# Kernel tuning notes

Measured on AMD Instinct MI355X. Metric: run time of the kernel, lower is better.

Reference implementation:

```python
import jax, jax.numpy as jnp
import numpy as np
import math

NP, MNP, BS, DIM, NH, TOPK, FF = 512, 4096, 8, 256, 8, 32, 2048
HD = DIM // NH
EPS = 1e-5


def _ln(x, w, b):
    mu = jnp.mean(x, axis=-1, keepdims=True)
    var = jnp.mean((x - mu) ** 2, axis=-1, keepdims=True)
    return (x - mu) / jnp.sqrt(var + EPS) * w + b


def _lin(x, w, b):
    return x @ w.T + b


def setup_inputs() -> dict:
    key = jax.random.key(0)
    ks = jax.random.split(key, 16)
    s = 0.02
    d = {
        "tgt": jax.random.normal(ks[0], (NP, BS, DIM), jnp.float32),
        "memory": jax.random.normal(ks[1], (MNP, BS, DIM), jnp.float32),
        "query_pos": jax.random.normal(ks[2], (NP, BS, DIM), jnp.float32),
        "key_pos": jax.random.normal(ks[3], (MNP, BS, DIM), jnp.float32),
        "cw1": jax.random.normal(ks[4], (DIM, DIM), jnp.float32) * s,
        "cb1": jnp.zeros((DIM,), jnp.float32),
        "cw2": jax.random.normal(ks[5], (DIM, DIM), jnp.float32) * s,
        "cb2": jnp.zeros((DIM,), jnp.float32),
        "cw3": jax.random.normal(ks[6], (DIM, DIM), jnp.float32) * s,
        "cb3": jnp.zeros((DIM,), jnp.float32),
        "sa_in_w": jax.random.normal(ks[7], (3 * DIM, DIM), jnp.float32) * s,
        "sa_in_b": jnp.zeros((3 * DIM,), jnp.float32),
        "sa_out_w": jax.random.normal(ks[8], (DIM, DIM), jnp.float32) * s,
        "sa_out_b": jnp.zeros((DIM,), jnp.float32),
        "ln1_w": jnp.ones((DIM,), jnp.float32),
        "ln1_b": jnp.zeros((DIM,), jnp.float32),
        "ln2_w": jnp.ones((DIM,), jnp.float32),
        "ln2_b": jnp.zeros((DIM,), jnp.float32),
        "ln3_w": jnp.ones((DIM,), jnp.float32),
        "ln3_b": jnp.zeros((DIM,), jnp.float32),
        "ff1_w": jax.random.normal(ks[9], (FF, DIM), jnp.float32) * s,
        "ff1_b": jnp.zeros((FF,), jnp.float32),
        "ff2_w": jax.random.normal(ks[10], (DIM, FF), jnp.float32) * s,
        "ff2_b": jnp.zeros((DIM,), jnp.float32),
    }
    return d


def _forward(tgt, memory, query_pos, key_pos,
             cw1, cb1, cw2, cb2, cw3, cb3,
             sa_in_w, sa_in_b, sa_out_w, sa_out_b,
             ln1_w, ln1_b, ln2_w, ln2_b, ln3_w, ln3_b,
             ff1_w, ff1_b, ff2_w, ff2_b):
    npq, bs, dim = tgt.shape
    mnp = memory.shape[0]
    scale = 1.0 / math.sqrt(HD)

    # --- top-k cosine similarity neighbor selection (indices, non-diff) ---
    x = tgt.transpose(1, 0, 2)        # [bs, np, dim]
    m = memory.transpose(1, 0, 2)     # [bs, mnp, dim]
    xn = x / jnp.linalg.norm(x, axis=2, keepdims=True)
    mn = m / jnp.linalg.norm(m, axis=2, keepdims=True)
    sim = jnp.einsum('bnd,bmd->bnm', xn, mn)          # [bs, np, mnp]
    _, rns = jax.lax.top_k(sim, TOPK)                  # [bs, np, topk]

    # --- masked cross attention ---
    qc = (tgt + query_pos).transpose(1, 0, 2)          # [bs, np, dim]
    kc = (memory + key_pos).transpose(1, 0, 2)         # [bs, mnp, dim]
    vc = m
    qh = _lin(qc, cw1, cb1).reshape(bs, npq, NH, HD).transpose(0, 2, 1, 3)   # [bs,nh,np,hd]
    kh = _lin(kc, cw2, cb2).reshape(bs, mnp, NH, HD).transpose(0, 2, 1, 3)   # [bs,nh,mnp,hd]
    vh = _lin(vc, cw3, cb3).reshape(bs, mnp, NH, HD).transpose(0, 2, 1, 3)   # [bs,nh,mnp,hd]
    w = jnp.einsum('bhnd,bhmd->bhnm', qh, kh) * scale                         # [bs,nh,np,mnp]

    b_idx = jnp.arange(bs)[:, None, None]
    n_idx = jnp.arange(npq)[None, :, None]
    mask = jnp.zeros((bs, npq, mnp), w.dtype).at[b_idx, n_idx, rns].set(1.0)  # same for all heads
    mask = mask[:, None, :, :]                                                # [bs,1,np,mnp]
    w = w * mask + (-1e9) * (1.0 - mask)
    w = jax.nn.softmax(w, axis=3)
    cross = jnp.einsum('bhnm,bhmd->bhnd', w, vh).transpose(2, 0, 1, 3).reshape(npq, bs, dim)

    t = _ln(tgt + cross, ln1_w, ln1_b)

    # --- self attention (torch nn.MultiheadAttention, q=k=t+pos, v=t) ---
    wq, wk, wv = sa_in_w[:DIM], sa_in_w[DIM:2 * DIM], sa_in_w[2 * DIM:]
    bq, bk, bv = sa_in_b[:DIM], sa_in_b[DIM:2 * DIM], sa_in_b[2 * DIM:]
    qk = t + query_pos                                 # [np, bs, dim]
    q2 = _lin(qk, wq, bq).transpose(1, 0, 2).reshape(bs, npq, NH, HD).transpose(0, 2, 1, 3)
    k2 = _lin(qk, wk, bk).transpose(1, 0, 2).reshape(bs, npq, NH, HD).transpose(0, 2, 1, 3)
    v2 = _lin(t, wv, bv).transpose(1, 0, 2).reshape(bs, npq, NH, HD).transpose(0, 2, 1, 3)
    attn = jax.nn.softmax(jnp.einsum('bhnd,bhmd->bhnm', q2, k2) * scale, axis=-1)
    sa = jnp.einsum('bhnm,bhmd->bhnd', attn, v2).transpose(2, 0, 1, 3).reshape(npq, bs, dim)
    sa = _lin(sa, sa_out_w, sa_out_b)

    t = _ln(t + sa, ln2_w, ln2_b)

    # --- FFN (exact GELU, matching torch F.gelu default) ---
    ff = _lin(jax.nn.gelu(_lin(t, ff1_w, ff1_b), approximate=False), ff2_w, ff2_b)
    t = _ln(t + ff, ln3_w, ln3_b)
    return t


def reference(tgt, memory, query_pos, key_pos,
              cw1, cb1, cw2, cb2, cw3, cb3,
              sa_in_w, sa_in_b, sa_out_w, sa_out_b,
              ln1_w, ln1_b, ln2_w, ln2_b, ln3_w, ln3_b,
              ff1_w, ff1_b, ff2_w, ff2_b):
    return _forward(tgt, memory, query_pos, key_pos,
                    cw1, cb1, cw2, cb2, cw3, cb3,
                    sa_in_w, sa_in_b, sa_out_w, sa_out_b,
                    ln1_w, ln1_b, ln2_w, ln2_b, ln3_w, ln3_b,
                    ff1_w, ff1_b, ff2_w, ff2_b)
```

## Files before the change

### kernel.cpp

```cpp
#include <hip/hip_runtime.h>
#include <math.h>

typedef unsigned short u16;
typedef unsigned int u32;
typedef __bf16 bf16x8 __attribute__((ext_vector_type(8)));
typedef float f32x4 __attribute__((ext_vector_type(4)));

#define NPQ 512
#define MNP 4096
#define BSZ 8
#define DIM 256
#define NH 8
#define HD 32
#define TOPK 32
#define FFD 2048
#define SCALE 0.17677669529663687f

__device__ __forceinline__ u16 f2bf(float f){
  u32 u = __builtin_bit_cast(u32, f);
  u = (u + 0x7FFFu + ((u >> 16) & 1u)) >> 16;
  return (u16)u;
}
__device__ __forceinline__ float bf2f(u16 h){
  u32 u = ((u32)h) << 16;
  return __builtin_bit_cast(float, u);
}
__device__ __forceinline__ float wredsum(float v){
#pragma unroll
  for (int m = 32; m; m >>= 1) v += __shfl_xor(v, m, 64);
  return v;
}
__device__ __forceinline__ float gelu_exact(float x){
  return 0.5f * x * (1.0f + erff(x * 0.70710678118654752f));
}
__device__ __forceinline__ u32 keytr(u32 u){
  return u ^ (((u32)((int)u >> 31)) | 0x80000000u);
}

__global__ __launch_bounds__(256)
void cvt_all(const float* __restrict__ s0, const float* __restrict__ s1,
             const float* __restrict__ s2, const float* __restrict__ s3,
             const float* __restrict__ s4, const float* __restrict__ s5,
             const float* __restrict__ s6, u16* __restrict__ dst){
  int i = blockIdx.x*256 + threadIdx.x;
  if (i >= 1507328) return;
  const float* s; int base;
  if      (i <  65536){ s = s0; base = 0; }
  else if (i < 131072){ s = s1; base = 65536; }
  else if (i < 196608){ s = s2; base = 131072; }
  else if (i < 393216){ s = s3; base = 196608; }
  else if (i < 458752){ s = s4; base = 393216; }
  else if (i < 983040){ s = s5; base = 458752; }
  else                { s = s6; base = 983040; }
  dst[i] = f2bf(s[i - base]);
}

__global__ __launch_bounds__(256)
void prep_tgt(const float* __restrict__ tgt, const float* __restrict__ qpos,
              u16* __restrict__ xnh, u16* __restrict__ xnl, u16* __restrict__ qc,
              const float* __restrict__ cb2, const float* __restrict__ cb3,
              float* __restrict__ cbKV){
  __shared__ float sc[4];
  int r = blockIdx.x, t = threadIdx.x;
  if (r == 0){ cbKV[t] = cb2[t]; cbKV[256 + t] = cb3[t]; }
  int b = r >> 9, n = r & 511;
  long src = ((long)n*BSZ + b)*DIM + t;
  float x = tgt[src];
  float s = wredsum(x*x);
  if ((t & 63) == 0) sc[t >> 6] = s;
  __syncthreads();
  float tot = sc[0]+sc[1]+sc[2]+sc[3];
  float xn = x / sqrtf(tot);
  u16 hi = f2bf(xn);
  long dst = (long)r*DIM + t;
  xnh[dst] = hi;
  xnl[dst] = f2bf(xn - bf2f(hi));
  qc[dst]  = f2bf(x + qpos[src]);
}

__global__ __launch_bounds__(256)
void prep_mem(const float* __restrict__ mem, const float* __restrict__ kpos,
              u16* __restrict__ mnh, u16* __restrict__ mnl,
              u16* __restrict__ kc, u16* __restrict__ vc){
  __shared__ float sc[4];
  int r = blockIdx.x, t = threadIdx.x;
  int b = r >> 12, mp = r & 4095;
  long src = ((long)mp*BSZ + b)*DIM + t;
  float x = mem[src];
  float s = wredsum(x*x);
  if ((t & 63) == 0) sc[t >> 6] = s;
  __syncthreads();
  float tot = sc[0]+sc[1]+sc[2]+sc[3];
  float xn = x / sqrtf(tot);
  u16 hi = f2bf(xn);
  long dst = (long)r*DIM + t;
  mnh[dst] = hi;
  mnl[dst] = f2bf(xn - bf2f(hi));
  kc[dst]  = f2bf(x + kpos[src]);
  vc[dst]  = f2bf(x);
}

#define BST 136
__global__ __launch_bounds__(256, 2)
void sim_gemm(const u16* __restrict__ xnh, const u16* __restrict__ xnl,
              const u16* __restrict__ mnh, const u16* __restrict__ mnl,
              float* __restrict__ sim){
  __shared__ __align__(16) u16 Bh[128*BST];
  __shared__ __align__(16) u16 Bl[128*BST];
  int t = threadIdx.x, lane = t & 63, wv = t >> 6;
  int ml = lane & 15, quad = lane >> 4;
  int b = blockIdx.z;
  int tM = blockIdx.y * 128 + (wv & 1) * 64;
  int tN = blockIdx.x * 128;
  int nloc = (wv >> 1) * 64;
  const u16* Ah = xnh + ((long)b*NPQ + tM + ml)*DIM;
  const u16* Al = xnl + ((long)b*NPQ + tM + ml)*DIM;
  f32x4 acc[4][4];
  f32x4 zer = {0.f,0.f,0.f,0.f};
#pragma unroll
  for (int i = 0; i < 4; i++)
#pragma unroll
    for (int j = 0; j < 4; j++) acc[i][j] = zer;

  int srow = t >> 4, scg = t & 15;
  for (int half = 0; half < 2; half++){
    int k0 = half * 128;
    if (half) __syncthreads();
#pragma unroll
    for (int p = 0; p < 8; p++){
      int r = p*16 + srow;
      long g = ((long)b*MNP + tN + r)*DIM + k0 + scg*8;
      *(uint4*)(&Bh[r*BST + scg*8]) = *(const uint4*)(mnh + g);
      *(uint4*)(&Bl[r*BST + scg*8]) = *(const uint4*)(mnl + g);
    }
    bf16x8 ca[4], ca2[4], na[4], na2[4];
#pragma unroll
    for (int i = 0; i < 4; i++){
      ca[i]  = *(const bf16x8*)(Ah + (long)i*16*DIM + k0 + quad*8);
      ca2[i] = *(const bf16x8*)(Al + (long)i*16*DIM + k0 + quad*8);
    }
    __syncthreads();
#pragma unroll
    for (int kk = 0; kk < 128; kk += 32){
      if (kk < 96){
#pragma unroll
        for (int i = 0; i < 4; i++){
          na[i]  = *(const bf16x8*)(Ah + (long)i*16*DIM + k0 + kk + 32 + quad*8);
          na2[i] = *(const bf16x8*)(Al + (long)i*16*DIM + k0 + kk + 32 + quad*8);
        }
      }
      bf16x8 bh[4], bl[4];
#pragma unroll
      for (int j = 0; j < 4; j++){
        int nr = nloc + j*16 + ml;
        bh[j] = *(const bf16x8*)(&Bh[nr*BST + kk + quad*8]);
        bl[j] = *(const bf16x8*)(&Bl[nr*BST + kk + quad*8]);
      }
#pragma unroll
      for (int i = 0; i < 4; i++)
#pragma unroll
        for (int j = 0; j < 4; j++){
          acc[i][j] = __builtin_amdgcn_mfma_f32_16x16x32_bf16(ca[i],  bh[j], acc[i][j], 0, 0, 0);
          acc[i][j] = __builtin_amdgcn_mfma_f32_16x16x32_bf16(ca[i],  bl[j], acc[i][j], 0, 0, 0);
          acc[i][j] = __builtin_amdgcn_mfma_f32_16x16x32_bf16(ca2[i], bh[j], acc[i][j], 0, 0, 0);
        }
#pragma unroll
      for (int i = 0; i < 4; i++){ ca[i] = na[i]; ca2[i] = na2[i]; }
    }
  }
  long zC = (long)b * NPQ * MNP;
#pragma unroll
  for (int i = 0; i < 4; i++)
#pragma unroll
    for (int r = 0; r < 4; r++){
      int row = tM + i*16 + quad*4 + r;
#pragma unroll
      for (int j = 0; j < 4; j++){
        int col = tN + nloc + j*16 + ml;
        sim[zC + (long)row*MNP + col] = acc[i][j][r];
      }
    }
}

#define PBST 264
template<int KGROUPS, int OUT_BF16, int ACT>
__global__ __launch_bounds__(256)
void pgemm(const u16* __restrict__ A, const u16* __restrict__ A2, int selCol,
           const u16* __restrict__ B, const float* __restrict__ bias,
           void* __restrict__ Cv, int N){
  __shared__ __align__(16) u16 Bs[64*PBST];
  const int K = KGROUPS*256;
  int t = threadIdx.x, lane = t & 63, wv = t >> 6;
  int ml = lane & 15, quad = lane >> 4;
  int tM = blockIdx.x*64;
  int tN = blockIdx.y*64;
  const u16* Ab = (tN < selCol) ? A : A2;
  const u16* Arow = Ab + (long)(tM + wv*16 + ml)*K;
  f32x4 acc[4];
  f32x4 zer = {0.f,0.f,0.f,0.f};
#pragma unroll
  for (int nj = 0; nj < 4; nj++) acc[nj] = zer;
  int srow = t >> 5, scol = (t & 31)*8;
  for (int g = 0; g < KGROUPS; g++){
    if (g) __syncthreads();
#pragma unroll
    for (int p = 0; p < 8; p++){
      int r = p*8 + srow;
      *(uint4*)(&Bs[r*PBST + scol]) = *(const uint4*)(B + (long)(tN + r)*K + g*256 + scol);
    }
    bf16x8 a[8];
#pragma unroll
    for (int kk = 0; kk < 8; kk++)
      a[kk] = *(const bf16x8*)(Arow + g*256 + kk*32 + quad*8);
    __syncthreads();
#pragma unroll
    for (int kk = 0; kk < 8; kk++){
#pragma unroll
      for (int nj = 0; nj < 4; nj++){
        bf16x8 bv = *(const bf16x8*)(&Bs[(nj*16 + ml)*PBST + kk*32 + quad*8]);
        acc[nj] = __builtin_amdgcn_mfma_f32_16x16x32_bf16(a[kk], bv, acc[nj], 0, 0, 0);
      }
    }
  }
#pragma unroll
  for (int nj = 0; nj < 4; nj++){
    int col = tN + nj*16 + ml;
    float bv = bias[col];
#pragma unroll
    for (int r = 0; r < 4; r++){
      int row = tM + wv*16 + quad*4 + r;
      float v = acc[nj][r] + bv;
      if (ACT == 1) v = gelu_exact(v);
      long idx = (long)row * N + col;
      if (OUT_BF16) ((u16*)Cv)[idx] = f2bf(v);
      else ((float*)Cv)[idx] = v;
    }
  }
}

#define HSTRIDE 264
__global__ __launch_bounds__(256, 4)
void topk_k(const float* __restrict__ sim, int* __restrict__ rns){
  __shared__ int hist[4*HSTRIDE];
  __shared__ int sh_B, sh_above;
  __shared__ int scnt, stcnt;
  __shared__ int sties[256];
  int t = threadIdx.x, wv = t >> 6;
  long r = blockIdx.x;
  const uint4* row4 = (const uint4*)(sim + r*4096);
  u32 key[16];
#pragma unroll
  for (int j = 0; j < 4; j++){
    uint4 v = row4[j*256 + t];
    key[j*4+0] = keytr(v.x);
    key[j*4+1] = keytr(v.y);
    key[j*4+2] = keytr(v.z);
    key[j*4+3] = keytr(v.w);
  }
#pragma unroll
  for (int i = 0; i < 16; i++) asm volatile("" : "+v"(key[i]));
  if (t == 0){ scnt = 0; stcnt = 0; }
  u32 pref = 0;
  int k_above = 0;
#pragma unroll 1
  for (int round = 0; round < 4; round++){
    int shift = 24 - round*8;
    u32 pmask = (round == 0) ? 0u : (0xFFFFFFFFu << (shift + 8));
    for (int z = t; z < 4*HSTRIDE; z += 256) hist[z] = 0;
    __syncthreads();
    int* myh = hist + wv*HSTRIDE;
#pragma unroll
    for (int i = 0; i < 16; i++){
      if (((key[i] ^ pref) & pmask) == 0)
        atomicAdd(&myh[(key[i] >> shift) & 255], 1);
    }
    __syncthreads();
    if (t < 64){
      int b0 = t*4+0, b1 = t*4+1, b2 = t*4+2, b3 = t*4+3;
      int h0 = hist[b0] + hist[HSTRIDE+b0] + hist[2*HSTRIDE+b0] + hist[3*HSTRIDE+b0];
      int h1 = hist[b1] + hist[HSTRIDE+b1] + hist[2*HSTRIDE+b1] + hist[3*HSTRIDE+b1];
      int h2 = hist[b2] + hist[HSTRIDE+b2] + hist[2*HSTRIDE+b2] + hist[3*HSTRIDE+b2];
      int h3 = hist[b3] + hist[HSTRIDE+b3] + hist[2*HSTRIDE+b3] + hist[3*HSTRIDE+b3];
      int local = h0 + h1 + h2 + h3;
      int s = local;
#pragma unroll
      for (int off = 1; off < 64; off <<= 1){
        int v = __shfl_down(s, off, 64);
        s += (t + off < 64) ? v : 0;
      }
      int excl = s - local;
      int a3 = excl, a2 = a3 + h3, a1 = a2 + h2, a0 = a1 + h1;
      int ka = k_above;
      if (ka + a3 < TOPK && ka + a3 + h3 >= TOPK){ sh_B = t*4+3; sh_above = ka + a3; }
      if (ka + a2 < TOPK && ka + a2 + h2 >= TOPK){ sh_B = t*4+2; sh_above = ka + a2; }
      if (ka + a1 < TOPK && ka + a1 + h1 >= TOPK){ sh_B = t*4+1; sh_above = ka + a1; }
      if (ka + a0 < TOPK && ka + a0 + h0 >= TOPK){ sh_B = t*4+0; sh_above = ka + a0; }
    }
    __syncthreads();
    pref |= ((u32)sh_B) << shift;
    k_above = sh_above;
  }
  int* out = rns + r*32;
#pragma unroll
  for (int i = 0; i < 16; i++){
    int gidx = (i >> 2)*1024 + t*4 + (i & 3);
    u32 kk = key[i];
    if (kk > pref){
      int p = atomicAdd(&scnt, 1);
      out[p] = gidx;
    } else if (kk == pref){
      int p = atomicAdd(&stcnt, 1);
      if (p < 256) sties[p] = gidx;
    }
  }
  __syncthreads();
  if (t == 0){
    int n = stcnt; if (n > 256) n = 256;
    int k_rem = TOPK - k_above;
    for (int s = 0; s < k_rem; s++){
      int mb = 0;
      for (int j = 1; j < n; j++) if (sties[j] < sties[mb]) mb = j;
      out[k_above + s] = sties[mb];
      sties[mb] = 0x7FFFFFFF;
    }
  }
}

#define CAS 272
__global__ __launch_bounds__(256)
void cross_attn(const u16* __restrict__ qh, const u16* __restrict__ khvh,
                const int* __restrict__ rns, float* __restrict__ crossO){
  __shared__ __align__(16) u16 Kg[32*CAS];
  __shared__ __align__(16) u16 Vg[32*CAS];
  __shared__ float qv[256];
  __shared__ int idxs[32];
  __shared__ float L[256];
  __shared__ float pm[8], ps[8];
  int r = blockIdx.x, t = threadIdx.x;
  int b = r >> 9;
  if (t < 32) idxs[t] = rns[(long)r*32 + t];
  qv[t] = bf2f(qh[(long)r*DIM + t]);
  __syncthreads();
  for (int i = t; i < 32*64; i += 256){
    int k = i >> 6, c = (i & 63) * 4;
    long src = ((long)b*MNP + idxs[k])*512 + c;
    *(ushort4*)(&Kg[k*CAS + c]) = *(const ushort4*)(khvh + src);
    *(ushort4*)(&Vg[k*CAS + c]) = *(const ushort4*)(khvh + src + 256);
  }
  __syncthreads();
  {
    int h = t >> 5, k = t & 31;
    float acc = 0.f;
#pragma unroll
    for (int d = 0; d < 32; d++) acc += qv[h*HD + d] * bf2f(Kg[k*CAS + h*HD + d]);
    L[t] = acc * SCALE;
  }
  __syncthreads();
  if (t < 8){
    float m = L[t*32];
    for (int k = 1; k < 32; k++) m = fmaxf(m, L[t*32 + k]);
    float s = 0.f;
    for (int k = 0; k < 32; k++) s += expf(L[t*32 + k] - m);
    pm[t] = m; ps[t] = s;
  }
  __syncthreads();
  {
    int h = t >> 5, dd = t & 31;
    float m = pm[h], inv = 1.0f/ps[h], acc = 0.f;
#pragma unroll
    for (int k = 0; k < 32; k++) acc += expf(L[h*32 + k] - m) * bf2f(Vg[k*CAS + h*HD + dd]);
    crossO[(long)r*DIM + t] = acc * inv;
  }
}

template<int MODE>
__global__ __launch_bounds__(256)
void ln_k(const float* __restrict__ xa, const float* __restrict__ xb,
          const float* __restrict__ qpos,
          const float* __restrict__ w, const float* __restrict__ bsh,
          float* __restrict__ yf, u16* __restrict__ yb, u16* __restrict__ qkb){
  __shared__ float sc[8];
  int r = blockIdx.x, t = threadIdx.x;
  int b = r >> 9, n = r & 511;
  long bidx = (long)r*DIM + t;
  long nidx = ((long)n*BSZ + b)*DIM + t;
  float x = (MODE == 1 ? xa[nidx] : xa[bidx]) + xb[bidx];
  float s  = wredsum(x);
  float s2 = wredsum(x*x);
  int wv = t >> 6;
  if ((t & 63) == 0){ sc[wv] = s; sc[4 + wv] = s2; }
  __syncthreads();
  float S  = sc[0]+sc[1]+sc[2]+sc[3];
  float S2 = sc[4]+sc[5]+sc[6]+sc[7];
  float mu  = S * (1.f/256.f);
  float var = S2 * (1.f/256.f) - mu*mu;
  float y = (x - mu) * (1.0f / sqrtf(var + 1e-5f)) * w[t] + bsh[t];
  if (MODE == 3){
    yf[nidx] = y;
  } else {
    yf[bidx] = y;
    yb[bidx] = f2bf(y);
    if (MODE == 1) qkb[bidx] = f2bf(y + qpos[nidx]);
  }
}

#define KST 40
#define PST 264
__global__ __launch_bounds__(256)
void self_attn(const u16* __restrict__ qkv, u16* __restrict__ sa_pre){
  __shared__ __align__(16) u16 KS[512*KST];
  __shared__ __align__(16) u16 QS[32*KST];
  __shared__ float mbuf[128];
  __shared__ float sbuf[128];
  u16* P  = KS;
  u16* Vt = KS + 32*PST;

  int qt = blockIdx.x, h = blockIdx.y, b = blockIdx.z;
  int t = threadIdx.x, lane = t & 63, wv = t >> 6;
  int ml = lane & 15, quad = lane >> 4;
  int n0 = qt * 32;

  {
    int q = t >> 3, d4 = (t & 7) * 4;
    const u16* src = qkv + ((long)b*NPQ + n0 + q)*768 + h*HD + d4;
    *(ushort2*)(QS + q*KST + d4)     = *(const ushort2*)(src);
    *(ushort2*)(QS + q*KST + d4 + 2) = *(const ushort2*)(src + 2);
  }
  for (int i = t; i < 512*8; i += 256){
    int j = i >> 3, d4 = (i & 7) * 4;
    const u16* src = qkv + ((long)b*NPQ + j)*768 + 256 + h*HD + d4;
    *(ushort2*)(KS + j*KST + d4)     = *(const ushort2*)(src);
    *(ushort2*)(KS + j*KST + d4 + 2) = *(const ushort2*)(src + 2);
  }
  __syncthreads();

  f32x4 acc[2][8];
  {
    bf16x8 aq[2];
#pragma unroll
    for (int mi = 0; mi < 2; mi++)
      aq[mi] = *(const bf16x8*)(QS + (mi*16 + ml)*KST + quad*8);
#pragma unroll
    for (int nj = 0; nj < 8; nj++){
      bf16x8 bk = *(const bf16x8*)(KS + (wv*128 + nj*16 + ml)*KST + quad*8);
      f32x4 z = {0.f,0.f,0.f,0.f};
#pragma unroll
      for (int mi = 0; mi < 2; mi++)
        acc[mi][nj] = __builtin_amdgcn_mfma_f32_16x16x32_bf16(aq[mi], bk, z, 0, 0, 0);
    }
  }
  float lmax[2][4];
#pragma unroll
  for (int mi = 0; mi < 2; mi++)
#pragma unroll
    for (int r = 0; r < 4; r++) lmax[mi][r] = -3.4e38f;
#pragma unroll
  for (int mi = 0; mi < 2; mi++)
#pragma unroll
    for (int nj = 0; nj < 8; nj++)
#pragma unroll
      for (int r = 0; r < 4; r++){
        float v = acc[mi][nj][r] * SCALE;
        acc[mi][nj][r] = v;
        lmax[mi][r] = fmaxf(lmax[mi][r], v);
      }
#pragma unroll
  for (int m = 1; m < 16; m <<= 1)
#pragma unroll
    for (int mi = 0; mi < 2; mi++)
#pragma unroll
      for (int r = 0; r < 4; r++)
        lmax[mi][r] = fmaxf(lmax[mi][r], __shfl_xor(lmax[mi][r], m, 64));
  if (ml == 0){
#pragma unroll
    for (int mi = 0; mi < 2; mi++)
#pragma unroll
      for (int r = 0; r < 4; r++)
        mbuf[(mi*16 + quad*4 + r)*4 + wv] = lmax[mi][r];
  }
  __syncthreads();
  float inv_[2][4];
  float lsum[2][4];
#pragma unroll
  for (int mi = 0; mi < 2; mi++)
#pragma unroll
    for (int r = 0; r < 4; r++){
      int row = mi*16 + quad*4 + r;
      float m0 = fmaxf(fmaxf(mbuf[row*4+0], mbuf[row*4+1]),
                       fmaxf(mbuf[row*4+2], mbuf[row*4+3]));
      float s = 0.f;
#pragma unroll
      for (int nj = 0; nj < 8; nj++){
        float e = __expf(acc[mi][nj][r] - m0);
        acc[mi][nj][r] = e;
        s += e;
      }
      lsum[mi][r] = s;
    }
#pragma unroll
  for (int m = 1; m < 16; m <<= 1)
#pragma unroll
    for (int mi = 0; mi < 2; mi++)
#pragma unroll
      for (int r = 0; r < 4; r++)
        lsum[mi][r] += __shfl_xor(lsum[mi][r], m, 64);
  if (ml == 0){
#pragma unroll
    for (int mi = 0; mi < 2; mi++)
#pragma unroll
      for (int r = 0; r < 4; r++)
        sbuf[(mi*16 + quad*4 + r)*4 + wv] = lsum[mi][r];
  }
  __syncthreads();
#pragma unroll
  for (int mi = 0; mi < 2; mi++)
#pragma unroll
    for (int r = 0; r < 4; r++){
      int row = mi*16 + quad*4 + r;
      inv_[mi][r] = 1.0f / (sbuf[row*4+0]+sbuf[row*4+1]+sbuf[row*4+2]+sbuf[row*4+3]);
    }

  int mi2 = wv >> 1, ni = wv & 1;
  f32x4 acc2 = {0.f,0.f,0.f,0.f};
  for (int half = 0; half < 2; half++){
    __syncthreads();
    if ((wv >> 1) == half){
      int cbase = (wv & 1) * 128;
#pragma unroll
      for (int mi = 0; mi < 2; mi++)
#pragma unroll
        for (int nj = 0; nj < 8; nj++)
#pragma unroll
          for (int r = 0; r < 4; r++)
            P[(mi*16 + quad*4 + r)*PST + cbase + nj*16 + ml] = f2bf(acc[mi][nj][r]);
    }
    for (int i = t; i < 2048; i += 256){
      int j = i >> 3, d4 = (i & 7) * 4;
      const u16* src = qkv + ((long)b*NPQ + half*256 + j)*768 + 512 + h*HD + d4;
      u16 v0 = src[0], v1 = src[1], v2e = src[2], v3 = src[3];
      Vt[(d4+0)*PST + j] = v0;
      Vt[(d4+1)*PST + j] = v1;
      Vt[(d4+2)*PST + j] = v2e;
      Vt[(d4+3)*PST + j] = v3;
    }
    __syncthreads();
#pragma unroll
    for (int k0 = 0; k0 < 256; k0 += 32){
      bf16x8 ap = *(const bf16x8*)(P  + (mi2*16 + ml)*PST + k0 + quad*8);
      bf16x8 bv = *(const bf16x8*)(Vt + (ni*16  + ml)*PST + k0 + quad*8);
      acc2 = __builtin_amdgcn_mfma_f32_16x16x32_bf16(ap, bv, acc2, 0, 0, 0);
    }
  }
#pragma unroll
  for (int r = 0; r < 4; r++){
    int row = mi2*16 + quad*4 + r;
    sa_pre[((long)b*NPQ + n0 + row)*DIM + h*HD + ni*16 + ml] =
        f2bf(acc2[r] * inv_[mi2][r]);
  }
}

extern "C" void kernel_launch(void* const* d_in, const int* in_sizes, int n_in,
                              void* d_out, int out_size, void* d_ws, size_t ws_size,
                              hipStream_t stream){
  (void)in_sizes; (void)n_in; (void)out_size; (void)ws_size;
  const float* tgt  = (const float*)d_in[0];
  const float* mem  = (const float*)d_in[1];
  const float* qpos = (const float*)d_in[2];
  const float* kpos = (const float*)d_in[3];
  const float* cw1  = (const float*)d_in[4];  const float* cb1 = (const float*)d_in[5];
  const float* cw2  = (const float*)d_in[6];  const float* cb2 = (const float*)d_in[7];
  const float* cw3  = (const float*)d_in[8];  const float* cb3 = (const float*)d_in[9];
  const float* saw  = (const float*)d_in[10]; const float* sab = (const float*)d_in[11];
  const float* sow  = (const float*)d_in[12]; const float* sob = (const float*)d_in[13];
  const float* ln1w = (const float*)d_in[14]; const float* ln1b = (const float*)d_in[15];
  const float* ln2w = (const float*)d_in[16]; const float* ln2b = (const float*)d_in[17];
  const float* ln3w = (const float*)d_in[18]; const float* ln3b = (const float*)d_in[19];
  const float* f1w  = (const float*)d_in[20]; const float* f1bs = (const float*)d_in[21];
  const float* f2w  = (const float*)d_in[22]; const float* f2bs = (const float*)d_in[23];

  char* base = (char*)d_ws;
  size_t off = 0;
  auto alloc = [&](size_t bytes) -> char* {
    char* p = base + off;
    off += (bytes + 255) & ~(size_t)255;
    return p;
  };
  u16* cw1b = (u16*)alloc(65536u*2);
  u16* cw2b = (u16*)alloc(65536u*2);
  u16* cw3b = (u16*)alloc(65536u*2);   (void)cw3b;
  u16* sawb = (u16*)alloc(196608u*2);
  u16* sowb = (u16*)alloc(65536u*2);
  u16* f1wb = (u16*)alloc(524288u*2);
  u16* f2wb = (u16*)alloc(524288u*2);
  int* rns  = (int*)alloc(4096u*32*4);
  float* cbKV = (float*)alloc(512*4);
  size_t offB = off;
  u16* xnh = (u16*)alloc((size_t)4096*256*2);
  u16* xnl = (u16*)alloc((size_t)4096*256*2);
  u16* mnh = (u16*)alloc((size_t)32768*256*2);
  u16* mnl = (u16*)alloc((size_t)32768*256*2);
  u16* qc  = (u16*)alloc((size_t)4096*256*2);
  u16* kc  = (u16*)alloc((size_t)32768*256*2);
  u16* vc  = (u16*)alloc((size_t)32768*256*2);
  float* sim = (float*)alloc((size_t)8*512*4096*4);

  char* regC = (char*)sim;
  u16* qh   = (u16*)regC;
  u16* khvh = (u16*)(regC + 2097152);
  char* regB = base + offB;
  size_t ob = 0;
  auto allocB = [&](size_t bytes) -> char* {
    char* p = regB + ob;
    ob += (bytes + 255) & ~(size_t)255;
    return p;
  };
  float* cross = (float*)allocB((size_t)4096*256*4);
  float* t1    = (float*)allocB((size_t)4096*256*4);
  u16*   t1b   = (u16*)allocB((size_t)4096*256*2);
  u16*   qkb   = (u16*)allocB((size_t)4096*256*2);
  u16*   qkv   = (u16*)allocB((size_t)4096*768*2);
  u16*   sa_pre= (u16*)allocB((size_t)4096*256*2);
  float* sa    = (float*)allocB((size_t)4096*256*4);
  float* t2    = (float*)allocB((size_t)4096*256*4);
  u16*   t2b   = (u16*)allocB((size_t)4096*256*2);
  u16*   h1    = (u16*)allocB((size_t)4096*2048*2);
  float* ff    = (float*)allocB((size_t)4096*256*4);

  const int BIG = 1 << 30;
  dim3 blk(256);
  cvt_all<<<dim3((1507328 + 255)/256), blk, 0, stream>>>(
      cw1, cw2, cw3, saw, sow, f1w, f2w, cw1b);
  prep_tgt<<<dim3(4096), blk, 0, stream>>>(tgt, qpos, xnh, xnl, qc, cb2, cb3, cbKV);
  prep_mem<<<dim3(32768), blk, 0, stream>>>(mem, kpos, mnh, mnl, kc, vc);
  sim_gemm<<<dim3(32,4,8), blk, 0, stream>>>(xnh, xnl, mnh, mnl, sim);
  topk_k<<<dim3(4096), blk, 0, stream>>>(sim, rns);
  pgemm<1,1,0><<<dim3(64,4), blk, 0, stream>>>(qc, qc, BIG, cw1b, cb1, qh, 256);
  pgemm<1,1,0><<<dim3(512,8), blk, 0, stream>>>(kc, vc, 256, cw2b, cbKV, khvh, 512);
  cross_attn<<<dim3(4096), blk, 0, stream>>>(qh, khvh, rns, cross);
  ln_k<1><<<dim3(4096), blk, 0, stream>>>(tgt, cross, qpos, ln1w, ln1b, t1, t1b, qkb);
  pgemm<1,1,0><<<dim3(64,12), blk, 0, stream>>>(qkb, t1b, 512, sawb, sab, qkv, 768);
  self_attn<<<dim3(16,8,8), blk, 0, stream>>>(qkv, sa_pre);
  pgemm<1,0,0><<<dim3(64,4), blk, 0, stream>>>(sa_pre, sa_pre, BIG, sowb, sob, sa, 256);
  ln_k<2><<<dim3(4096), blk, 0, stream>>>(t1, sa, nullptr, ln2w, ln2b, t2, t2b, nullptr);
  pgemm<1,1,1><<<dim3(64,32), blk, 0, stream>>>(t2b, t2b, BIG, f1wb, f1bs, h1, 2048);
  pgemm<8,0,0><<<dim3(64,4), blk, 0, stream>>>(h1, h1, BIG, f2wb, f2bs, ff, 256);
  ln_k<3><<<dim3(4096), blk, 0, stream>>>(t2, ff, nullptr, ln3w, ln3b, (float*)d_out, nullptr, nullptr);
}
```

Baseline: 427.6 us.

## Merge prep kernels and co-schedule top-k with K/V/Q projections in one launch

Three preprocessing kernels (weight conversion, target prep, memory prep) become one launch that dispatches on block index. Top-k selection and the Q and K/V projection GEMMs are merged into one heterogeneous kernel, so the bandwidth-bound top-k runs alongside the compute-bound projections. This needs separate buffers for qh and khvh instead of aliasing the sim buffer, so it depends on workspace size and falls back to the old path otherwise. The merged kernel uses the larger shared-memory footprint and occupancy hint of the two, which may reduce top-k occupancy.

Result: no change. 427.1 us (-0.1%).

```diff
diff --git a/kernel.cpp b/kernel.cpp
--- a/kernel.cpp
+++ b/kernel.cpp
@@ -37,67 +37,68 @@
   return u ^ (((u32)((int)u >> 31)) | 0x80000000u);
 }
 
+#define FP_MEM_B 32768
+#define FP_TGT_B (32768 + 4096)
+#define FP_TOT_B (32768 + 4096 + 5888)
 __global__ __launch_bounds__(256)
-void cvt_all(const float* __restrict__ s0, const float* __restrict__ s1,
-             const float* __restrict__ s2, const float* __restrict__ s3,
-             const float* __restrict__ s4, const float* __restrict__ s5,
-             const float* __restrict__ s6, u16* __restrict__ dst){
-  int i = blockIdx.x*256 + threadIdx.x;
-  if (i >= 1507328) return;
-  const float* s; int base;
-  if      (i <  65536){ s = s0; base = 0; }
-  else if (i < 131072){ s = s1; base = 65536; }
-  else if (i < 196608){ s = s2; base = 131072; }
-  else if (i < 393216){ s = s3; base = 196608; }
-  else if (i < 458752){ s = s4; base = 393216; }
-  else if (i < 983040){ s = s5; base = 458752; }
-  else                { s = s6; base = 983040; }
-  dst[i] = f2bf(s[i - base]);
-}
-
-__global__ __launch_bounds__(256)
-void prep_tgt(const float* __restrict__ tgt, const float* __restrict__ qpos,
-              u16* __restrict__ xnh, u16* __restrict__ xnl, u16* __restrict__ qc,
-              const float* __restrict__ cb2, const float* __restrict__ cb3,
-              float* __restrict__ cbKV){
+void fused_prep(const float* __restrict__ mem, const float* __restrict__ kpos,
+                u16* __restrict__ mnh, u16* __restrict__ mnl,
+                u16* __restrict__ kc, u16* __restrict__ vc,
+                const float* __restrict__ tgt, const float* __restrict__ qpos,
+                u16* __restrict__ xnh, u16* __restrict__ xnl, u16* __restrict__ qc,
+                const float* __restrict__ cb2, const float* __restrict__ cb3,
+                float* __restrict__ cbKV,
+                const float* __restrict__ s0, const float* __restrict__ s1,
+                const float* __restrict__ s2, const float* __restrict__ s3,
+                const float* __restrict__ s4, const float* __restrict__ s5,
+                const float* __restrict__ s6, u16* __restrict__ wdst){
   __shared__ float sc[4];
-  int r = blockIdx.x, t = threadIdx.x;
-  if (r == 0){ cbKV[t] = cb2[t]; cbKV[256 + t] = cb3[t]; }
-  int b = r >> 9, n = r & 511;
-  long src = ((long)n*BSZ + b)*DIM + t;
-  float x = tgt[src];
-  float s = wredsum(x*x);
-  if ((t & 63) == 0) sc[t >> 6] = s;
-  __syncthreads();
-  float tot = sc[0]+sc[1]+sc[2]+sc[3];
-  float xn = x / sqrtf(tot);
-  u16 hi = f2bf(xn);
-  long dst = (long)r*DIM + t;
-  xnh[dst] = hi;
-  xnl[dst] = f2bf(xn - bf2f(hi));
-  qc[dst]  = f2bf(x + qpos[src]);
-}
-
-__global__ __launch_bounds__(256)
-void prep_mem(const float* __restrict__ mem, const float* __restrict__ kpos,
-              u16* __restrict__ mnh, u16* __restrict__ mnl,
-              u16* __restrict__ kc, u16* __restrict__ vc){
-  __shared__ float sc[4];
-  int r = blockIdx.x, t = threadIdx.x;
-  int b = r >> 12, mp = r & 4095;
-  long src = ((long)mp*BSZ + b)*DIM + t;
-  float x = mem[src];
-  float s = wredsum(x*x);
-  if ((t & 63) == 0) sc[t >> 6] = s;
-  __syncthreads();
-  float tot = sc[0]+sc[1]+sc[2]+sc[3];
-  float xn = x / sqrtf(tot);
-  u16 hi = f2bf(xn);
-  long dst = (long)r*DIM + t;
-  mnh[dst] = hi;
-  mnl[dst] = f2bf(xn - bf2f(hi));
-  kc[dst]  = f2bf(x + kpos[src]);
-  vc[dst]  = f2bf(x);
+  int gb = blockIdx.x, t = threadIdx.x;
+  if (gb < FP_MEM_B){
+    int r = gb;
+    int b = r >> 12, mp = r & 4095;
+    long src = ((long)mp*BSZ + b)*DIM + t;
+    float x = mem[src];
+    float s = wredsum(x*x);
+    if ((t & 63) == 0) sc[t >> 6] = s;
+    __syncthreads();
+    float tot = sc[0]+sc[1]+sc[2]+sc[3];
+    float xn = x / sqrtf(tot);
+    u16 hi = f2bf(xn);
+    long dst = (long)r*DIM + t;
+    mnh[dst] = hi;
+    mnl[dst] = f2bf(xn - bf2f(hi));
+    kc[dst]  = f2bf(x + kpos[src]);
+    vc[dst]  = f2bf(x);
+  } else if (gb < FP_TGT_B){
+    int r = gb - FP_MEM_B;
+    if (r == 0){ cbKV[t] = cb2[t]; cbKV[256 + t] = cb3[t]; }
+    int b = r >> 9, n = r & 511;
+    long src = ((long)n*BSZ + b)*DIM + t;
+    float x = tgt[src];
+    float s = wredsum(x*x);
+    if ((t & 63) == 0) sc[t >> 6] = s;
+    __syncthreads();
+    float tot = sc[0]+sc[1]+sc[2]+sc[3];
+    float xn = x / sqrtf(tot);
+    u16 hi = f2bf(xn);
+    long dst = (long)r*DIM + t;
+    xnh[dst] = hi;
+    xnl[dst] = f2bf(xn - bf2f(hi));
+    qc[dst]  = f2bf(x + qpos[src]);
+  } else {
+    int i = (gb - FP_TGT_B)*256 + t;
+    if (i >= 1507328) return;
+    const float* s; int base;
+    if      (i <  65536){ s = s0; base = 0; }
+    else if (i < 131072){ s = s1; base = 65536; }
+    else if (i < 196608){ s = s2; base = 131072; }
+    else if (i < 393216){ s = s3; base = 196608; }
+    else if (i < 458752){ s = s4; base = 393216; }
+    else if (i < 983040){ s = s5; base = 458752; }
+    else                { s = s6; base = 983040; }
+    wdst[i] = f2bf(s[i - base]);
+  }
 }
 
 #define BST 136
@@ -184,16 +185,13 @@
 
 #define PBST 264
 template<int KGROUPS, int OUT_BF16, int ACT>
-__global__ __launch_bounds__(256)
-void pgemm(const u16* __restrict__ A, const u16* __restrict__ A2, int selCol,
-           const u16* __restrict__ B, const float* __restrict__ bias,
-           void* __restrict__ Cv, int N){
-  __shared__ __align__(16) u16 Bs[64*PBST];
+__device__ __forceinline__
+void pgemm_body(const u16* __restrict__ A, const u16* __restrict__ A2, int selCol,
+                const u16* __restrict__ B, const float* __restrict__ bias,
+                void* __restrict__ Cv, int N, int tM, int tN, u16* Bs){
   const int K = KGROUPS*256;
   int t = threadIdx.x, lane = t & 63, wv = t >> 6;
   int ml = lane & 15, quad = lane >> 4;
-  int tM = blockIdx.x*64;
-  int tN = blockIdx.y*64;
   const u16* Ab = (tN < selCol) ? A : A2;
   const u16* Arow = Ab + (long)(tM + wv*16 + ml)*K;
   f32x4 acc[4];
@@ -238,15 +236,25 @@
   }
 }
 
+template<int KGROUPS, int OUT_BF16, int ACT>
+__global__ __launch_bounds__(256)
+void pgemm(const u16* __restrict__ A, const u16* __restrict__ A2, int selCol,
+           const u16* __restrict__ B, const float* __restrict__ bias,
+           void* __restrict__ Cv, int N){
+  __shared__ __align__(16) u16 Bs[64*PBST];
+  pgemm_body<KGROUPS,OUT_BF16,ACT>(A, A2, selCol, B, bias, Cv, N,
+                                   blockIdx.x*64, blockIdx.y*64, Bs);
+}
+
 #define HSTRIDE 264
-__global__ __launch_bounds__(256, 4)
-void topk_k(const float* __restrict__ sim, int* __restrict__ rns){
-  __shared__ int hist[4*HSTRIDE];
-  __shared__ int sh_B, sh_above;
-  __shared__ int scnt, stcnt;
-  __shared__ int sties[256];
+#define TK_SMEM (4*HSTRIDE*4 + 1024 + 16)
+__device__ __forceinline__
+void topk_body(const float* __restrict__ sim, int* __restrict__ rns,
+               long r, char* smem){
+  int* hist  = (int*)smem;
+  int* sties = (int*)(smem + 4*HSTRIDE*4);
+  int* sc4   = (int*)(smem + 4*HSTRIDE*4 + 1024);
   int t = threadIdx.x, wv = t >> 6;
-  long r = blockIdx.x;
   const uint4* row4 = (const uint4*)(sim + r*4096);
   u32 key[16];
 #pragma unroll
@@ -259,7 +267,7 @@
   }
 #pragma unroll
   for (int i = 0; i < 16; i++) asm volatile("" : "+v"(key[i]));
-  if (t == 0){ scnt = 0; stcnt = 0; }
+  if (t == 0){ sc4[2] = 0; sc4[3] = 0; }
   u32 pref = 0;
   int k_above = 0;
 #pragma unroll 1
@@ -291,14 +299,14 @@
       int excl = s - local;
       int a3 = excl, a2 = a3 + h3, a1 = a2 + h2, a0 = a1 + h1;
       int ka = k_above;
-      if (ka + a3 < TOPK && ka + a3 + h3 >= TOPK){ sh_B = t*4+3; sh_above = ka + a3; }
-      if (ka + a2 < TOPK && ka + a2 + h2 >= TOPK){ sh_B = t*4+2; sh_above = ka + a2; }
-      if (ka + a1 < TOPK && ka + a1 + h1 >= TOPK){ sh_B = t*4+1; sh_above = ka + a1; }
-      if (ka + a0 < TOPK && ka + a0 + h0 >= TOPK){ sh_B = t*4+0; sh_above = ka + a0; }
-    }
-    __syncthreads();
-    pref |= ((u32)sh_B) << shift;
-    k_above = sh_above;
+      if (ka + a3 < TOPK && ka + a3 + h3 >= TOPK){ sc4[0] = t*4+3; sc4[1] = ka + a3; }
+      if (ka + a2 < TOPK && ka + a2 + h2 >= TOPK){ sc4[0] = t*4+2; sc4[1] = ka + a2; }
+      if (ka + a1 < TOPK && ka + a1 + h1 >= TOPK){ sc4[0] = t*4+1; sc4[1] = ka + a1; }
+      if (ka + a0 < TOPK && ka + a0 + h0 >= TOPK){ sc4[0] = t*4+0; sc4[1] = ka + a0; }
+    }
+    __syncthreads();
+    pref |= ((u32)sc4[0]) << shift;
+    k_above = sc4[1];
   }
   int* out = rns + r*32;
 #pragma unroll
@@ -306,16 +314,16 @@
     int gidx = (i >> 2)*1024 + t*4 + (i & 3);
     u32 kk = key[i];
     if (kk > pref){
-      int p = atomicAdd(&scnt, 1);
+      int p = atomicAdd(&sc4[2], 1);
       out[p] = gidx;
     } else if (kk == pref){
-      int p = atomicAdd(&stcnt, 1);
+      int p = atomicAdd(&sc4[3], 1);
       if (p < 256) sties[p] = gidx;
     }
   }
   __syncthreads();
   if (t == 0){
-    int n = stcnt; if (n > 256) n = 256;
+    int n = sc4[3]; if (n > 256) n = 256;
     int k_rem = TOPK - k_above;
     for (int s = 0; s < k_rem; s++){
       int mb = 0;
@@ -323,6 +331,38 @@
       out[k_above + s] = sties[mb];
       sties[mb] = 0x7FFFFFFF;
     }
+  }
+}
+
+__global__ __launch_bounds__(256, 4)
+void topk_k(const float* __restrict__ sim, int* __restrict__ rns){
+  __shared__ __align__(16) char smem[TK_SMEM];
+  topk_body(sim, rns, blockIdx.x, smem);
+}
+
+#define FM_SMEM (64*PBST*2)
+#define FM_QH_B   (4096)
+#define FM_KHVH_B (4096 + 256)
+#define FM_TOT_B  (4096 + 256 + 4096)
+__global__ __launch_bounds__(256, 3)
+void fused_mid(const float* __restrict__ sim, int* __restrict__ rns,
+               const u16* __restrict__ qc, const u16* __restrict__ cw1b,
+               const float* __restrict__ cb1, u16* __restrict__ qh,
+               const u16* __restrict__ kc, const u16* __restrict__ vc,
+               const u16* __restrict__ cw2b, const float* __restrict__ cbKV,
+               u16* __restrict__ khvh){
+  __shared__ __align__(16) char smem[FM_SMEM];
+  int gb = blockIdx.x;
+  if (gb < FM_QH_B){
+    topk_body(sim, rns, gb, smem);
+  } else if (gb < FM_KHVH_B){
+    int id = gb - FM_QH_B;
+    pgemm_body<1,1,0>(qc, qc, 1 << 30, cw1b, cb1, qh, 256,
+                      (id & 63)*64, (id >> 6)*64, (u16*)smem);
+  } else {
+    int id = gb - FM_KHVH_B;
+    pgemm_body<1,1,0>(kc, vc, 256, cw2b, cbKV, khvh, 512,
+                      (id & 511)*64, (id >> 9)*64, (u16*)smem);
   }
 }
 
@@ -562,7 +602,7 @@
 extern "C" void kernel_launch(void* const* d_in, const int* in_sizes, int n_in,
                               void* d_out, int out_size, void* d_ws, size_t ws_size,
                               hipStream_t stream){
-  (void)in_sizes; (void)n_in; (void)out_size; (void)ws_size;
+  (void)in_sizes; (void)n_in; (void)out_size;
   const float* tgt  = (const float*)d_in[0];
   const float* mem  = (const float*)d_in[1];
   const float* qpos = (const float*)d_in[2];
@@ -604,9 +644,19 @@
   u16* vc  = (u16*)alloc((size_t)32768*256*2);
   float* sim = (float*)alloc((size_t)8*512*4096*4);
 
-  char* regC = (char*)sim;
-  u16* qh   = (u16*)regC;
-  u16* khvh = (u16*)(regC + 2097152);
+  const size_t QH_BYTES = (size_t)4096*256*2;
+  const size_t KHVH_BYTES = (size_t)32768*512*2;
+  bool fusedMid = (ws_size >= off + QH_BYTES + KHVH_BYTES + 1024);
+  u16 *qh, *khvh;
+  if (fusedMid){
+    qh   = (u16*)alloc(QH_BYTES);
+    khvh = (u16*)alloc(KHVH_BYTES);
+  } else {
+    char* regC = (char*)sim;
+    qh   = (u16*)regC;
+    khvh = (u16*)(regC + 2097152);
+  }
+
   char* regB = base + offB;
   size_t ob = 0;
   auto allocB = [&](size_t bytes) -> char* {
@@ -628,14 +678,19 @@
 
   const int BIG = 1 << 30;
   dim3 blk(256);
-  cvt_all<<<dim3((1507328 + 255)/256), blk, 0, stream>>>(
+  fused_prep<<<dim3(FP_TOT_B), blk, 0, stream>>>(
+      mem, kpos, mnh, mnl, kc, vc,
+      tgt, qpos, xnh, xnl, qc, cb2, cb3, cbKV,
       cw1, cw2, cw3, saw, sow, f1w, f2w, cw1b);
-  prep_tgt<<<dim3(4096), blk, 0, stream>>>(tgt, qpos, xnh, xnl, qc, cb2, cb3, cbKV);
-  prep_mem<<<dim3(32768), blk, 0, stream>>>(mem, kpos, mnh, mnl, kc, vc);
   sim_gemm<<<dim3(32,4,8), blk, 0, stream>>>(xnh, xnl, mnh, mnl, sim);
-  topk_k<<<dim3(4096), blk, 0, stream>>>(sim, rns);
-  pgemm<1,1,0><<<dim3(64,4), blk, 0, stream>>>(qc, qc, BIG, cw1b, cb1, qh, 256);
-  pgemm<1,1,0><<<dim3(512,8), blk, 0, stream>>>(kc, vc, 256, cw2b, cbKV, khvh, 512);
+  if (fusedMid){
+    fused_mid<<<dim3(FM_TOT_B), blk, 0, stream>>>(
+        sim, rns, qc, cw1b, cb1, qh, kc, vc, cw2b, cbKV, khvh);
+  } else {
+    topk_k<<<dim3(4096), blk, 0, stream>>>(sim, rns);
+    pgemm<1,1,0><<<dim3(64,4), blk, 0, stream>>>(qc, qc, BIG, cw1b, cb1, qh, 256);
+    pgemm<1,1,0><<<dim3(512,8), blk, 0, stream>>>(kc, vc, 256, cw2b, cbKV, khvh, 512);
+  }
   cross_attn<<<dim3(4096), blk, 0, stream>>>(qh, khvh, rns, cross);
   ln_k<1><<<dim3(4096), blk, 0, stream>>>(tgt, cross, qpos, ln1w, ln1b, t1, t1b, qkb);
   pgemm<1,1,0><<<dim3(64,12), blk, 0, stream>>>(qkb, t1b, 512, sawb, sab, qkv, 768);
```

## Fuse prep kernels into one launch and aggregate topk histogram atomics per wave

Applied to the files above, without the earlier changes.

Merges the weight conversion, target prep and memory prep kernels into a single launch whose blocks branch on their index, removing two launch boundaries and their tails. In the top-k histogram pass, each wave now uses ballot and shuffle to group lanes that hit the same bin and issues one atomic per distinct bin instead of one per lane. This cuts LDS atomic contention when many keys share a bucket, especially in later radix rounds. The cost is a serial loop over distinct bins, which may be slow when bins are spread out, as in the first round.

After: 458.8 us. 7.3% more time.

```diff
diff --git a/kernel.cpp b/kernel.cpp
--- a/kernel.cpp
+++ b/kernel.cpp
@@ -37,67 +37,68 @@
   return u ^ (((u32)((int)u >> 31)) | 0x80000000u);
 }
 
+#define FP_MEM_B 32768
+#define FP_TGT_B (32768 + 4096)
+#define FP_TOT_B (32768 + 4096 + 5888)
 __global__ __launch_bounds__(256)
-void cvt_all(const float* __restrict__ s0, const float* __restrict__ s1,
-             const float* __restrict__ s2, const float* __restrict__ s3,
-             const float* __restrict__ s4, const float* __restrict__ s5,
-             const float* __restrict__ s6, u16* __restrict__ dst){
-  int i = blockIdx.x*256 + threadIdx.x;
-  if (i >= 1507328) return;
-  const float* s; int base;
-  if      (i <  65536){ s = s0; base = 0; }
-  else if (i < 131072){ s = s1; base = 65536; }
-  else if (i < 196608){ s = s2; base = 131072; }
-  else if (i < 393216){ s = s3; base = 196608; }
-  else if (i < 458752){ s = s4; base = 393216; }
-  else if (i < 983040){ s = s5; base = 458752; }
-  else                { s = s6; base = 983040; }
-  dst[i] = f2bf(s[i - base]);
-}
-
-__global__ __launch_bounds__(256)
-void prep_tgt(const float* __restrict__ tgt, const float* __restrict__ qpos,
-              u16* __restrict__ xnh, u16* __restrict__ xnl, u16* __restrict__ qc,
-              const float* __restrict__ cb2, const float* __restrict__ cb3,
-              float* __restrict__ cbKV){
+void fused_prep(const float* __restrict__ mem, const float* __restrict__ kpos,
+                u16* __restrict__ mnh, u16* __restrict__ mnl,
+                u16* __restrict__ kc, u16* __restrict__ vc,
+                const float* __restrict__ tgt, const float* __restrict__ qpos,
+                u16* __restrict__ xnh, u16* __restrict__ xnl, u16* __restrict__ qc,
+                const float* __restrict__ cb2, const float* __restrict__ cb3,
+                float* __restrict__ cbKV,
+                const float* __restrict__ s0, const float* __restrict__ s1,
+                const float* __restrict__ s2, const float* __restrict__ s3,
+                const float* __restrict__ s4, const float* __restrict__ s5,
+                const float* __restrict__ s6, u16* __restrict__ wdst){
   __shared__ float sc[4];
-  int r = blockIdx.x, t = threadIdx.x;
-  if (r == 0){ cbKV[t] = cb2[t]; cbKV[256 + t] = cb3[t]; }
-  int b = r >> 9, n = r & 511;
-  long src = ((long)n*BSZ + b)*DIM + t;
-  float x = tgt[src];
-  float s = wredsum(x*x);
-  if ((t & 63) == 0) sc[t >> 6] = s;
-  __syncthreads();
-  float tot = sc[0]+sc[1]+sc[2]+sc[3];
-  float xn = x / sqrtf(tot);
-  u16 hi = f2bf(xn);
-  long dst = (long)r*DIM + t;
-  xnh[dst] = hi;
-  xnl[dst] = f2bf(xn - bf2f(hi));
-  qc[dst]  = f2bf(x + qpos[src]);
-}
-
-__global__ __launch_bounds__(256)
-void prep_mem(const float* __restrict__ mem, const float* __restrict__ kpos,
-              u16* __restrict__ mnh, u16* __restrict__ mnl,
-              u16* __restrict__ kc, u16* __restrict__ vc){
-  __shared__ float sc[4];
-  int r = blockIdx.x, t = threadIdx.x;
-  int b = r >> 12, mp = r & 4095;
-  long src = ((long)mp*BSZ + b)*DIM + t;
-  float x = mem[src];
-  float s = wredsum(x*x);
-  if ((t & 63) == 0) sc[t >> 6] = s;
-  __syncthreads();
-  float tot = sc[0]+sc[1]+sc[2]+sc[3];
-  float xn = x / sqrtf(tot);
-  u16 hi = f2bf(xn);
-  long dst = (long)r*DIM + t;
-  mnh[dst] = hi;
-  mnl[dst] = f2bf(xn - bf2f(hi));
-  kc[dst]  = f2bf(x + kpos[src]);
-  vc[dst]  = f2bf(x);
+  int gb = blockIdx.x, t = threadIdx.x;
+  if (gb < FP_MEM_B){
+    int r = gb;
+    int b = r >> 12, mp = r & 4095;
+    long src = ((long)mp*BSZ + b)*DIM + t;
+    float x = mem[src];
+    float s = wredsum(x*x);
+    if ((t & 63) == 0) sc[t >> 6] = s;
+    __syncthreads();
+    float tot = sc[0]+sc[1]+sc[2]+sc[3];
+    float xn = x / sqrtf(tot);
+    u16 hi = f2bf(xn);
+    long dst = (long)r*DIM + t;
+    mnh[dst] = hi;
+    mnl[dst] = f2bf(xn - bf2f(hi));
+    kc[dst]  = f2bf(x + kpos[src]);
+    vc[dst]  = f2bf(x);
+  } else if (gb < FP_TGT_B){
+    int r = gb - FP_MEM_B;
+    if (r == 0){ cbKV[t] = cb2[t]; cbKV[256 + t] = cb3[t]; }
+    int b = r >> 9, n = r & 511;
+    long src = ((long)n*BSZ + b)*DIM + t;
+    float x = tgt[src];
+    float s = wredsum(x*x);
+    if ((t & 63) == 0) sc[t >> 6] = s;
+    __syncthreads();
+    float tot = sc[0]+sc[1]+sc[2]+sc[3];
+    float xn = x / sqrtf(tot);
+    u16 hi = f2bf(xn);
+    long dst = (long)r*DIM + t;
+    xnh[dst] = hi;
+    xnl[dst] = f2bf(xn - bf2f(hi));
+    qc[dst]  = f2bf(x + qpos[src]);
+  } else {
+    int i = (gb - FP_TGT_B)*256 + t;
+    if (i >= 1507328) return;
+    const float* s; int base;
+    if      (i <  65536){ s = s0; base = 0; }
+    else if (i < 131072){ s = s1; base = 65536; }
+    else if (i < 196608){ s = s2; base = 131072; }
+    else if (i < 393216){ s = s3; base = 196608; }
+    else if (i < 458752){ s = s4; base = 393216; }
+    else if (i < 983040){ s = s5; base = 458752; }
+    else                { s = s6; base = 983040; }
+    wdst[i] = f2bf(s[i - base]);
+  }
 }
 
 #define BST 136
@@ -245,7 +246,7 @@
   __shared__ int sh_B, sh_above;
   __shared__ int scnt, stcnt;
   __shared__ int sties[256];
-  int t = threadIdx.x, wv = t >> 6;
+  int t = threadIdx.x, wv = t >> 6, lane = t & 63;
   long r = blockIdx.x;
   const uint4* row4 = (const uint4*)(sim + r*4096);
   u32 key[16];
@@ -269,10 +270,18 @@
     for (int z = t; z < 4*HSTRIDE; z += 256) hist[z] = 0;
     __syncthreads();
     int* myh = hist + wv*HSTRIDE;
-#pragma unroll
+#pragma unroll 1
     for (int i = 0; i < 16; i++){
-      if (((key[i] ^ pref) & pmask) == 0)
-        atomicAdd(&myh[(key[i] >> shift) & 255], 1);
+      bool pred = ((key[i] ^ pref) & pmask) == 0;
+      u32 d = (key[i] >> shift) & 255;
+      unsigned long long todo = __ballot(pred);
+      while (todo){
+        int src = (int)__builtin_ctzll(todo);
+        u32 dd = __shfl(d, src, 64);
+        unsigned long long match = __ballot(pred && d == dd);
+        if (lane == src) atomicAdd(&myh[dd], (int)__popcll(match));
+        todo &= ~match;
+      }
     }
     __syncthreads();
     if (t < 64){
@@ -628,10 +637,10 @@
 
   const int BIG = 1 << 30;
   dim3 blk(256);
-  cvt_all<<<dim3((1507328 + 255)/256), blk, 0, stream>>>(
+  fused_prep<<<dim3(FP_TOT_B), blk, 0, stream>>>(
+      mem, kpos, mnh, mnl, kc, vc,
+      tgt, qpos, xnh, xnl, qc, cb2, cb3, cbKV,
       cw1, cw2, cw3, saw, sow, f1w, f2w, cw1b);
-  prep_tgt<<<dim3(4096), blk, 0, stream>>>(tgt, qpos, xnh, xnl, qc, cb2, cb3, cbKV);
-  prep_mem<<<dim3(32768), blk, 0, stream>>>(mem, kpos, mnh, mnl, kc, vc);
   sim_gemm<<<dim3(32,4,8), blk, 0, stream>>>(xnh, xnl, mnh, mnl, sim);
   topk_k<<<dim3(4096), blk, 0, stream>>>(sim, rns);
   pgemm<1,1,0><<<dim3(64,4), blk, 0, stream>>>(qc, qc, BIG, cw1b, cb1, qh, 256);
```
